# Performance work log

Measured on AMD Instinct MI355X. Metric: run time of the kernel, lower is better.

## Reference

```python
import jax, jax.numpy as jnp
import numpy as np

HIDDEN = 128
D_T = 128
D_S = 128
EPS = 1e-3  # keras LayerNormalization default epsilon


def setup_inputs() -> dict:
    key = jax.random.key(0)
    ks = jax.random.split(key, 9)
    B, S = 1024, 1024
    h_t = jax.random.normal(ks[0], (B, D_T), dtype=jnp.float32)
    h_s = jax.random.normal(ks[1], (B, S, D_S), dtype=jnp.float32)
    # Dense kernels (keras Dense: y = x @ W + b)
    W_a = jax.random.normal(ks[2], (D_T, HIDDEN), dtype=jnp.float32) * (1.0 / np.sqrt(D_T))
    U_a = jax.random.normal(ks[3], (D_S, HIDDEN), dtype=jnp.float32) * (1.0 / np.sqrt(D_S))
    V_a = jax.random.normal(ks[4], (HIDDEN, 1), dtype=jnp.float32) * (1.0 / np.sqrt(HIDDEN))
    W_c = jax.random.normal(ks[5], (D_S + D_T, HIDDEN), dtype=jnp.float32) * (1.0 / np.sqrt(D_S + D_T))
    b_c = jnp.zeros((HIDDEN,), dtype=jnp.float32)
    gamma = jnp.ones((HIDDEN,), dtype=jnp.float32)
    beta = jnp.zeros((HIDDEN,), dtype=jnp.float32)
    return {"h_t": h_t, "h_s": h_s, "W_a": W_a, "U_a": U_a, "V_a": V_a,
            "W_c": W_c, "b_c": b_c, "gamma": gamma, "beta": beta}


def reference(h_t, h_s, W_a, U_a, V_a, W_c, b_c, gamma, beta):
    # Additive (Bahdanau) attention scores
    ht_proj = h_t @ W_a                              # [B, H]
    hs_proj = jnp.einsum('bsd,dh->bsh', h_s, U_a)    # [B, S, H]
    energy = jnp.tanh(hs_proj + ht_proj[:, None, :])  # [B, S, H]
    scores = jnp.einsum('bsh,ho->bso', energy, V_a)  # [B, S, 1]
    alpha = jax.nn.softmax(scores, axis=1)           # softmax over sequence
    context = jnp.sum(alpha * h_s, axis=1)           # [B, D_S]
    concat = jnp.concatenate([context, h_t], axis=-1)  # [B, D_S + D_T]
    attn_vec = jnp.tanh(concat @ W_c + b_c)          # [B, H]
    # LayerNorm over last axis (keras default eps=1e-3)
    mu = jnp.mean(attn_vec, axis=-1, keepdims=True)
    var = jnp.mean(jnp.square(attn_vec - mu), axis=-1, keepdims=True)
    out = (attn_vec - mu) * jax.lax.rsqrt(var + EPS) * gamma + beta
    return out
```

## Files before the change

### kernel.cpp

```cpp
#include <hip/hip_runtime.h>

#define SEQ 1024
#define TS  64
#define NT  (SEQ/TS)

typedef unsigned short u16;
typedef unsigned int   u32;
typedef __bf16 bf16x8 __attribute__((ext_vector_type(8)));
typedef float  f32x4  __attribute__((ext_vector_type(4)));

__device__ __forceinline__ u16 f2bf(float f) {
    u32 u = __float_as_uint(f);
    u += 0x7fffu + ((u >> 16) & 1u);
    return (u16)(u >> 16);
}
__device__ __forceinline__ float bf2f(u16 h) {
    return __uint_as_float(((u32)h) << 16);
}
__device__ __forceinline__ float fast_tanh(float x) {
    float e = __expf(x + x);
    return 1.0f - 2.0f * __builtin_amdgcn_rcpf(e + 1.0f);
}

__global__ __launch_bounds__(256, 3)
void attn_fused(const float* __restrict__ h_t, const float* __restrict__ h_s,
                const float* __restrict__ W_a, const float* __restrict__ U_a,
                const float* __restrict__ V_a, const float* __restrict__ W_c,
                const float* __restrict__ b_c, const float* __restrict__ gamma,
                const float* __restrict__ beta, float* __restrict__ out)
{
    __shared__ u16 Ut[128*128];
    __shared__ u16 tileB[TS*128];
    __shared__ float htp[128];
    __shared__ float Vs[128];
    __shared__ float htrow[128];
    __shared__ float redArr[4*16];
    __shared__ float cw[4*128];
    __shared__ float mw[4], lw[4];
    __shared__ float lnp[4], lnq[4];

    const int tid = threadIdx.x;
    const int b   = blockIdx.x;
    const int w   = tid >> 6, l = tid & 63;
    const int lo  = l & 15,  hi = l >> 4;

    if (tid < 128) {
        htrow[tid] = h_t[b*128 + tid];
        Vs[tid]    = V_a[tid];
    }

    const float4* U4 = (const float4*)U_a;
    #pragma unroll
    for (int i = 0; i < 16; ++i) {
        int f4i = i*256 + tid;
        float4 v = U4[f4i];
        int k  = f4i >> 5;
        int cb = (f4i & 31) * 4;
        float vv[4] = {v.x, v.y, v.z, v.w};
        #pragma unroll
        for (int j = 0; j < 4; ++j) {
            int c = cb + j;
            Ut[c*128 + (((k>>3) ^ (c&7)) << 3) + (k&7)] = f2bf(vv[j]);
        }
    }
    __syncthreads();

    const float4* hs4 = (const float4*)h_s + (size_t)b * (SEQ*128/4);

    float4 rr[8];
    #pragma unroll
    for (int i = 0; i < 8; ++i) rr[i] = hs4[i*256 + tid];

    if (tid < 128) {
        float acc = 0.f;
        #pragma unroll 4
        for (int d = 0; d < 128; ++d) acc += htrow[d] * W_a[d*128 + tid];
        htp[tid] = acc;
    }

    #pragma unroll
    for (int i = 0; i < 8; ++i) {
        int f4i = i*256 + tid;
        int row = f4i >> 5, cf4 = f4i & 31;
        ushort4 pk = { f2bf(rr[i].x), f2bf(rr[i].y), f2bf(rr[i].z), f2bf(rr[i].w) };
        *(ushort4*)&tileB[row*128 + (((cf4>>1) ^ (row&7))<<3) + ((cf4&1)<<2)] = pk;
    }
    __syncthreads();

    float htpR[8], VsR[8];
    #pragma unroll
    for (int n = 0; n < 8; ++n) { htpR[n] = htp[n*16 + lo]; VsR[n] = Vs[n*16 + lo]; }

    const int swz = lo & 7;
    int aOff[4], bOff[4];
    #pragma unroll
    for (int ks = 0; ks < 4; ++ks) {
        int blk = (((ks*4 + hi) ^ swz) << 3);
        aOff[ks] = (w*16 + lo)*128 + blk;
        bOff[ks] = lo*128 + blk;
    }
    const int cblk   = l >> 2;
    const int ctxOff = (l & 3) << 1;

    float m = -1e30f, lsum = 0.f, c0 = 0.f, c1 = 0.f;

    for (int tt = 0; tt < NT; ++tt) {
        if (tt < NT-1) {
            #pragma unroll
            for (int i = 0; i < 8; ++i) rr[i] = hs4[(tt+1)*2048 + i*256 + tid];
        }

        bf16x8 a0 = *(const bf16x8*)&tileB[aOff[0]];
        bf16x8 a1 = *(const bf16x8*)&tileB[aOff[1]];
        bf16x8 a2 = *(const bf16x8*)&tileB[aOff[2]];
        bf16x8 a3 = *(const bf16x8*)&tileB[aOff[3]];
        float part0 = 0.f, part1 = 0.f, part2 = 0.f, part3 = 0.f;
        #pragma unroll
        for (int n = 0; n < 8; ++n) {
            f32x4 acc = {0.f, 0.f, 0.f, 0.f};
            acc = __builtin_amdgcn_mfma_f32_16x16x32_bf16(a0, *(const bf16x8*)&Ut[n*2048 + bOff[0]], acc, 0, 0, 0);
            acc = __builtin_amdgcn_mfma_f32_16x16x32_bf16(a1, *(const bf16x8*)&Ut[n*2048 + bOff[1]], acc, 0, 0, 0);
            acc = __builtin_amdgcn_mfma_f32_16x16x32_bf16(a2, *(const bf16x8*)&Ut[n*2048 + bOff[2]], acc, 0, 0, 0);
            acc = __builtin_amdgcn_mfma_f32_16x16x32_bf16(a3, *(const bf16x8*)&Ut[n*2048 + bOff[3]], acc, 0, 0, 0);
            float hC = htpR[n], vC = VsR[n];
            part0 += fast_tanh(acc[0] + hC) * vC;
            part1 += fast_tanh(acc[1] + hC) * vC;
            part2 += fast_tanh(acc[2] + hC) * vC;
            part3 += fast_tanh(acc[3] + hC) * vC;
        }
        #pragma unroll
        for (int msk = 1; msk < 16; msk <<= 1) {
            part0 += __shfl_xor(part0, msk);
            part1 += __shfl_xor(part1, msk);
            part2 += __shfl_xor(part2, msk);
            part3 += __shfl_xor(part3, msk);
        }
        float tm = fmaxf(fmaxf(part0, part1), fmaxf(part2, part3));
        tm = fmaxf(tm, __shfl_xor(tm, 16));
        tm = fmaxf(tm, __shfl_xor(tm, 32));
        float nm = fmaxf(m, tm);
        float sc = __expf(m - nm);
        c0 *= sc; c1 *= sc; lsum *= sc; m = nm;
        float w0 = __expf(part0 - m), w1 = __expf(part1 - m);
        float w2 = __expf(part2 - m), w3 = __expf(part3 - m);
        lsum += w0 + w1 + w2 + w3;
        if (lo == 0) {
            redArr[w*16 + hi*4 + 0] = w0;
            redArr[w*16 + hi*4 + 1] = w1;
            redArr[w*16 + hi*4 + 2] = w2;
            redArr[w*16 + hi*4 + 3] = w3;
        }
        #pragma unroll
        for (int r = 0; r < 16; ++r) {
            float wr = redArr[w*16 + r];
            u32 ud = *(const u32*)&tileB[(w*16 + r)*128 + ((cblk ^ (r&7)) << 3) + ctxOff];
            c0 += wr * bf2f((u16)(ud & 0xffffu));
            c1 += wr * bf2f((u16)(ud >> 16));
        }
        __syncthreads();
        if (tt < NT-1) {
            #pragma unroll
            for (int i = 0; i < 8; ++i) {
                int f4i = i*256 + tid;
                int row = f4i >> 5, cf4 = f4i & 31;
                ushort4 pk = { f2bf(rr[i].x), f2bf(rr[i].y), f2bf(rr[i].z), f2bf(rr[i].w) };
                *(ushort4*)&tileB[row*128 + (((cf4>>1) ^ (row&7))<<3) + ((cf4&1)<<2)] = pk;
            }
        }
        __syncthreads();
    }

    float lt = lsum;
    lt += __shfl_xor(lt, 16);
    lt += __shfl_xor(lt, 32);
    if (l == 0) { mw[w] = m; lw[w] = lt; }
    cw[w*128 + 2*l]     = c0;
    cw[w*128 + 2*l + 1] = c1;
    __syncthreads();

    if (tid < 128) {
        float M = fmaxf(fmaxf(mw[0], mw[1]), fmaxf(mw[2], mw[3]));
        float L = 0.f, C = 0.f;
        #pragma unroll
        for (int wv = 0; wv < 4; ++wv) {
            float s = __expf(mw[wv] - M);
            L += lw[wv] * s;
            C += cw[wv*128 + tid] * s;
        }
        htp[tid] = C / L;
    }
    __syncthreads();

    float av = 0.f;
    if (tid < 128) {
        float acc = b_c[tid];
        #pragma unroll 4
        for (int k = 0; k < 128; ++k) acc += htp[k]   * W_c[k*128 + tid];
        #pragma unroll 4
        for (int k = 0; k < 128; ++k) acc += htrow[k] * W_c[(128 + k)*128 + tid];
        av = fast_tanh(acc);
    }
    float s1 = (tid < 128) ? av : 0.f;
    #pragma unroll
    for (int msk = 1; msk < 64; msk <<= 1) s1 += __shfl_xor(s1, msk);
    if (l == 0) lnp[w] = s1;
    __syncthreads();
    float mu  = (lnp[0] + lnp[1]) * (1.f/128.f);
    float dev = av - mu;
    float s2 = (tid < 128) ? dev*dev : 0.f;
    #pragma unroll
    for (int msk = 1; msk < 64; msk <<= 1) s2 += __shfl_xor(s2, msk);
    if (l == 0) lnq[w] = s2;
    __syncthreads();
    float var = (lnq[0] + lnq[1]) * (1.f/128.f);
    if (tid < 128) {
        out[b*128 + tid] = dev * rsqrtf(var + 1e-3f) * gamma[tid] + beta[tid];
    }
}

extern "C" void kernel_launch(void* const* d_in, const int* in_sizes, int n_in,
                              void* d_out, int out_size, void* d_ws, size_t ws_size,
                              hipStream_t stream) {
    const float* h_t  = (const float*)d_in[0];
    const float* h_s  = (const float*)d_in[1];
    const float* W_a  = (const float*)d_in[2];
    const float* U_a  = (const float*)d_in[3];
    const float* V_a  = (const float*)d_in[4];
    const float* W_c  = (const float*)d_in[5];
    const float* b_c  = (const float*)d_in[6];
    const float* gam  = (const float*)d_in[7];
    const float* bet  = (const float*)d_in[8];
    float* out = (float*)d_out;
    hipLaunchKernelGGL(attn_fused, dim3(1024), dim3(256), 0, stream,
                       h_t, h_s, W_a, U_a, V_a, W_c, b_c, gam, bet, out);
}
```

Measured before the change: 155.8 us.

## Double-buffer h_s register prefetch two tiles ahead and use native bf16 conversion

Uses two register buffers for h_s tiles, loading each tile two iterations before it is committed to LDS, so global-load latency gets more compute time to hide behind. The loop is unrolled by two with macros. The manual float-to-bf16 rounding is replaced by the compiler's native __bf16 cast, which may map to hardware convert instructions. The extra 32 float registers per thread raise register pressure under the 3-blocks-per-SM launch bound and could cause spills or lower occupancy.

```diff
diff --git a/kernel.cpp b/kernel.cpp
--- a/kernel.cpp
+++ b/kernel.cpp
@@ -7,13 +7,9 @@
 typedef unsigned short u16;
 typedef unsigned int   u32;
 typedef __bf16 bf16x8 __attribute__((ext_vector_type(8)));
+typedef __bf16 bf16x4 __attribute__((ext_vector_type(4)));
 typedef float  f32x4  __attribute__((ext_vector_type(4)));
 
-__device__ __forceinline__ u16 f2bf(float f) {
-    u32 u = __float_as_uint(f);
-    u += 0x7fffu + ((u >> 16) & 1u);
-    return (u16)(u >> 16);
-}
 __device__ __forceinline__ float bf2f(u16 h) {
     return __uint_as_float(((u32)h) << 16);
 }
@@ -21,6 +17,76 @@
     float e = __expf(x + x);
     return 1.0f - 2.0f * __builtin_amdgcn_rcpf(e + 1.0f);
 }
+
+#define LOADT(rr, tt)                                                   \
+    do {                                                                \
+        _Pragma("unroll")                                               \
+        for (int i = 0; i < 8; ++i) rr[i] = hs4[(tt)*2048 + i*256 + tid]; \
+    } while (0)
+
+#define COMMIT(rr)                                                      \
+    do {                                                                \
+        _Pragma("unroll")                                               \
+        for (int i = 0; i < 8; ++i) {                                   \
+            int f4i = i*256 + tid;                                      \
+            int row = f4i >> 5, cf4 = f4i & 31;                         \
+            bf16x4 pk;                                                  \
+            pk[0] = (__bf16)rr[i].x; pk[1] = (__bf16)rr[i].y;           \
+            pk[2] = (__bf16)rr[i].z; pk[3] = (__bf16)rr[i].w;           \
+            *(bf16x4*)&tileB[row*128 + (((cf4>>1) ^ (row&7))<<3) + ((cf4&1)<<2)] = pk; \
+        }                                                               \
+    } while (0)
+
+#define COMPUTE()                                                       \
+    do {                                                                \
+        bf16x8 a0 = *(const bf16x8*)&tileB[aOff[0]];                    \
+        bf16x8 a1 = *(const bf16x8*)&tileB[aOff[1]];                    \
+        bf16x8 a2 = *(const bf16x8*)&tileB[aOff[2]];                    \
+        bf16x8 a3 = *(const bf16x8*)&tileB[aOff[3]];                    \
+        float part0 = 0.f, part1 = 0.f, part2 = 0.f, part3 = 0.f;       \
+        _Pragma("unroll")                                               \
+        for (int n = 0; n < 8; ++n) {                                   \
+            f32x4 acc = {0.f, 0.f, 0.f, 0.f};                           \
+            acc = __builtin_amdgcn_mfma_f32_16x16x32_bf16(a0, *(const bf16x8*)&Ut[n*2048 + bOff[0]], acc, 0, 0, 0); \
+            acc = __builtin_amdgcn_mfma_f32_16x16x32_bf16(a1, *(const bf16x8*)&Ut[n*2048 + bOff[1]], acc, 0, 0, 0); \
+            acc = __builtin_amdgcn_mfma_f32_16x16x32_bf16(a2, *(const bf16x8*)&Ut[n*2048 + bOff[2]], acc, 0, 0, 0); \
+            acc = __builtin_amdgcn_mfma_f32_16x16x32_bf16(a3, *(const bf16x8*)&Ut[n*2048 + bOff[3]], acc, 0, 0, 0); \
+            float hC = htpR[n], vC = VsR[n];                            \
+            part0 += fast_tanh(acc[0] + hC) * vC;                       \
+            part1 += fast_tanh(acc[1] + hC) * vC;                       \
+            part2 += fast_tanh(acc[2] + hC) * vC;                       \
+            part3 += fast_tanh(acc[3] + hC) * vC;                       \
+        }                                                               \
+        _Pragma("unroll")                                               \
+        for (int msk = 1; msk < 16; msk <<= 1) {                        \
+            part0 += __shfl_xor(part0, msk);                            \
+            part1 += __shfl_xor(part1, msk);                            \
+            part2 += __shfl_xor(part2, msk);                            \
+            part3 += __shfl_xor(part3, msk);                            \
+        }                                                               \
+        float tm = fmaxf(fmaxf(part0, part1), fmaxf(part2, part3));     \
+        tm = fmaxf(tm, __shfl_xor(tm, 16));                             \
+        tm = fmaxf(tm, __shfl_xor(tm, 32));                             \
+        float nm = fmaxf(m, tm);                                        \
+        float sc = __expf(m - nm);                                      \
+        c0 *= sc; c1 *= sc; lsum *= sc; m = nm;                         \
+        float w0 = __expf(part0 - m), w1 = __expf(part1 - m);           \
+        float w2 = __expf(part2 - m), w3 = __expf(part3 - m);           \
+        lsum += w0 + w1 + w2 + w3;                                      \
+        if (lo == 0) {                                                  \
+            redArr[w*16 + hi*4 + 0] = w0;                               \
+            redArr[w*16 + hi*4 + 1] = w1;                               \
+            redArr[w*16 + hi*4 + 2] = w2;                               \
+            redArr[w*16 + hi*4 + 3] = w3;                               \
+        }                                                               \
+        _Pragma("unroll")                                               \
+        for (int r = 0; r < 16; ++r) {                                  \
+            float wr = redArr[w*16 + r];                                \
+            u32 ud = *(const u32*)&tileB[(w*16 + r)*128 + ((cblk ^ (r&7)) << 3) + ctxOff]; \
+            c0 += wr * bf2f((u16)(ud & 0xffffu));                       \
+            c1 += wr * bf2f((u16)(ud >> 16));                           \
+        }                                                               \
+    } while (0)
 
 __global__ __launch_bounds__(256, 3)
 void attn_fused(const float* __restrict__ h_t, const float* __restrict__ h_s,
@@ -60,16 +126,16 @@
         #pragma unroll
         for (int j = 0; j < 4; ++j) {
             int c = cb + j;
-            Ut[c*128 + (((k>>3) ^ (c&7)) << 3) + (k&7)] = f2bf(vv[j]);
+            Ut[c*128 + (((k>>3) ^ (c&7)) << 3) + (k&7)] = __builtin_bit_cast(u16, (__bf16)vv[j]);
         }
     }
     __syncthreads();
 
     const float4* hs4 = (const float4*)h_s + (size_t)b * (SEQ*128/4);
 
-    float4 rr[8];
-    #pragma unroll
-    for (int i = 0; i < 8; ++i) rr[i] = hs4[i*256 + tid];
+    float4 rrA[8], rrB[8];
+    LOADT(rrA, 0);
+    LOADT(rrB, 1);
 
     if (tid < 128) {
         float acc = 0.f;
@@ -78,13 +144,7 @@
         htp[tid] = acc;
     }
 
-    #pragma unroll
-    for (int i = 0; i < 8; ++i) {
-        int f4i = i*256 + tid;
-        int row = f4i >> 5, cf4 = f4i & 31;
-        ushort4 pk = { f2bf(rr[i].x), f2bf(rr[i].y), f2bf(rr[i].z), f2bf(rr[i].w) };
-        *(ushort4*)&tileB[row*128 + (((cf4>>1) ^ (row&7))<<3) + ((cf4&1)<<2)] = pk;
-    }
+    COMMIT(rrA);
     __syncthreads();
 
     float htpR[8], VsR[8];
@@ -104,69 +164,17 @@
 
     float m = -1e30f, lsum = 0.f, c0 = 0.f, c1 = 0.f;
 
-    for (int tt = 0; tt < NT; ++tt) {
-        if (tt < NT-1) {
-            #pragma unroll
-            for (int i = 0; i < 8; ++i) rr[i] = hs4[(tt+1)*2048 + i*256 + tid];
-        }
-
-        bf16x8 a0 = *(const bf16x8*)&tileB[aOff[0]];
-        bf16x8 a1 = *(const bf16x8*)&tileB[aOff[1]];
-        bf16x8 a2 = *(const bf16x8*)&tileB[aOff[2]];
-        bf16x8 a3 = *(const bf16x8*)&tileB[aOff[3]];
-        float part0 = 0.f, part1 = 0.f, part2 = 0.f, part3 = 0.f;
-        #pragma unroll
-        for (int n = 0; n < 8; ++n) {
-            f32x4 acc = {0.f, 0.f, 0.f, 0.f};
-            acc = __builtin_amdgcn_mfma_f32_16x16x32_bf16(a0, *(const bf16x8*)&Ut[n*2048 + bOff[0]], acc, 0, 0, 0);
-            acc = __builtin_amdgcn_mfma_f32_16x16x32_bf16(a1, *(const bf16x8*)&Ut[n*2048 + bOff[1]], acc, 0, 0, 0);
-            acc = __builtin_amdgcn_mfma_f32_16x16x32_bf16(a2, *(const bf16x8*)&Ut[n*2048 + bOff[2]], acc, 0, 0, 0);
-            acc = __builtin_amdgcn_mfma_f32_16x16x32_bf16(a3, *(const bf16x8*)&Ut[n*2048 + bOff[3]], acc, 0, 0, 0);
-            float hC = htpR[n], vC = VsR[n];
-            part0 += fast_tanh(acc[0] + hC) * vC;
-            part1 += fast_tanh(acc[1] + hC) * vC;
-            part2 += fast_tanh(acc[2] + hC) * vC;
-            part3 += fast_tanh(acc[3] + hC) * vC;
-        }
-        #pragma unroll
-        for (int msk = 1; msk < 16; msk <<= 1) {
-            part0 += __shfl_xor(part0, msk);
-            part1 += __shfl_xor(part1, msk);
-            part2 += __shfl_xor(part2, msk);
-            part3 += __shfl_xor(part3, msk);
-        }
-        float tm = fmaxf(fmaxf(part0, part1), fmaxf(part2, part3));
-        tm = fmaxf(tm, __shfl_xor(tm, 16));
-        tm = fmaxf(tm, __shfl_xor(tm, 32));
-        float nm = fmaxf(m, tm);
-        float sc = __expf(m - nm);
-        c0 *= sc; c1 *= sc; lsum *= sc; m = nm;
-        float w0 = __expf(part0 - m), w1 = __expf(part1 - m);
-        float w2 = __expf(part2 - m), w3 = __expf(part3 - m);
-        lsum += w0 + w1 + w2 + w3;
-        if (lo == 0) {
-            redArr[w*16 + hi*4 + 0] = w0;
-            redArr[w*16 + hi*4 + 1] = w1;
-            redArr[w*16 + hi*4 + 2] = w2;
-            redArr[w*16 + hi*4 + 3] = w3;
-        }
-        #pragma unroll
-        for (int r = 0; r < 16; ++r) {
-            float wr = redArr[w*16 + r];
-            u32 ud = *(const u32*)&tileB[(w*16 + r)*128 + ((cblk ^ (r&7)) << 3) + ctxOff];
-            c0 += wr * bf2f((u16)(ud & 0xffffu));
-            c1 += wr * bf2f((u16)(ud >> 16));
-        }
-        __syncthreads();
-        if (tt < NT-1) {
-            #pragma unroll
-            for (int i = 0; i < 8; ++i) {
-                int f4i = i*256 + tid;
-                int row = f4i >> 5, cf4 = f4i & 31;
-                ushort4 pk = { f2bf(rr[i].x), f2bf(rr[i].y), f2bf(rr[i].z), f2bf(rr[i].w) };
-                *(ushort4*)&tileB[row*128 + (((cf4>>1) ^ (row&7))<<3) + ((cf4&1)<<2)] = pk;
-            }
-        }
+    for (int t = 0; t < NT; t += 2) {
+        if (t + 2 < NT) LOADT(rrA, t + 2);
+        COMPUTE();
+        __syncthreads();
+        COMMIT(rrB);
+        __syncthreads();
+
+        if (t + 3 < NT) LOADT(rrB, t + 3);
+        COMPUTE();
+        __syncthreads();
+        if (t + 2 < NT) COMMIT(rrA);
         __syncthreads();
     }
 
```

Result: slower. 368.6 us (+136.6%).

## Hold U_a fragments in registers and double-buffer per-wave h_s tiles without barriers

Applied to the files above, without the earlier changes.

Each thread now keeps its slice of the U_a MFMA B-operand in registers as bf16 fragments, so the 32 KB shared-memory copy of U_a and its per-tile LDS reads go away. Each wave loads and stores only its own 16 rows of h_s into a double-buffered shared tile, which removes both __syncthreads from the main loop. The bf16 conversion uses the native cast instead of manual rounding. The cost is much higher register pressure (launch bounds lowered from 3 to 2 blocks per CU) and strided uncoalesced global reads of U_a per block.

```diff
diff --git a/kernel.cpp b/kernel.cpp
--- a/kernel.cpp
+++ b/kernel.cpp
@@ -1,19 +1,15 @@
 #include <hip/hip_runtime.h>
 
 #define SEQ 1024
-#define TS  64
-#define NT  (SEQ/TS)
+#define NT  16
+#define TILE_U16 (64*128)
 
 typedef unsigned short u16;
 typedef unsigned int   u32;
 typedef __bf16 bf16x8 __attribute__((ext_vector_type(8)));
+typedef __bf16 bf16x4 __attribute__((ext_vector_type(4)));
 typedef float  f32x4  __attribute__((ext_vector_type(4)));
 
-__device__ __forceinline__ u16 f2bf(float f) {
-    u32 u = __float_as_uint(f);
-    u += 0x7fffu + ((u >> 16) & 1u);
-    return (u16)(u >> 16);
-}
 __device__ __forceinline__ float bf2f(u16 h) {
     return __uint_as_float(((u32)h) << 16);
 }
@@ -22,54 +18,120 @@
     return 1.0f - 2.0f * __builtin_amdgcn_rcpf(e + 1.0f);
 }
 
-__global__ __launch_bounds__(256, 3)
+#define LOADT(rr, tt)                                                       \
+    do {                                                                    \
+        _Pragma("unroll")                                                   \
+        for (int i = 0; i < 8; ++i)                                         \
+            rr[i] = hs4[(tt)*2048 + w*512 + i*64 + l];                      \
+    } while (0)
+
+#define COMMIT(rr, sel)                                                     \
+    do {                                                                    \
+        _Pragma("unroll")                                                   \
+        for (int i = 0; i < 8; ++i) {                                       \
+            int f4i = i*64 + l;                                             \
+            int r   = w*16 + (f4i >> 5);                                    \
+            int cf4 = f4i & 31;                                             \
+            bf16x4 pk;                                                      \
+            pk[0] = (__bf16)rr[i].x; pk[1] = (__bf16)rr[i].y;               \
+            pk[2] = (__bf16)rr[i].z; pk[3] = (__bf16)rr[i].w;               \
+            *(bf16x4*)&tileB[(sel)*TILE_U16 + r*128 +                       \
+                             (((cf4>>1) ^ (r&7))<<3) + ((cf4&1)<<2)] = pk;  \
+        }                                                                   \
+    } while (0)
+
+#define COMPUTE(sel)                                                        \
+    do {                                                                    \
+        const u16* tb = &tileB[(sel)*TILE_U16];                             \
+        bf16x8 a0 = *(const bf16x8*)&tb[aOff[0]];                           \
+        bf16x8 a1 = *(const bf16x8*)&tb[aOff[1]];                           \
+        bf16x8 a2 = *(const bf16x8*)&tb[aOff[2]];                           \
+        bf16x8 a3 = *(const bf16x8*)&tb[aOff[3]];                           \
+        float part0 = 0.f, part1 = 0.f, part2 = 0.f, part3 = 0.f;           \
+        _Pragma("unroll")                                                   \
+        for (int n = 0; n < 8; ++n) {                                       \
+            f32x4 acc = {0.f, 0.f, 0.f, 0.f};                               \
+            acc = __builtin_amdgcn_mfma_f32_16x16x32_bf16(a0, Bf[n][0], acc, 0, 0, 0); \
+            acc = __builtin_amdgcn_mfma_f32_16x16x32_bf16(a1, Bf[n][1], acc, 0, 0, 0); \
+            acc = __builtin_amdgcn_mfma_f32_16x16x32_bf16(a2, Bf[n][2], acc, 0, 0, 0); \
+            acc = __builtin_amdgcn_mfma_f32_16x16x32_bf16(a3, Bf[n][3], acc, 0, 0, 0); \
+            float hC = htpR[n], vC = VsR[n];                                \
+            part0 += fast_tanh(acc[0] + hC) * vC;                           \
+            part1 += fast_tanh(acc[1] + hC) * vC;                           \
+            part2 += fast_tanh(acc[2] + hC) * vC;                           \
+            part3 += fast_tanh(acc[3] + hC) * vC;                           \
+        }                                                                   \
+        _Pragma("unroll")                                                   \
+        for (int msk = 1; msk < 16; msk <<= 1) {                            \
+            part0 += __shfl_xor(part0, msk);                                \
+            part1 += __shfl_xor(part1, msk);                                \
+            part2 += __shfl_xor(part2, msk);                                \
+            part3 += __shfl_xor(part3, msk);                                \
+        }                                                                   \
+        float tm = fmaxf(fmaxf(part0, part1), fmaxf(part2, part3));         \
+        tm = fmaxf(tm, __shfl_xor(tm, 16));                                 \
+        tm = fmaxf(tm, __shfl_xor(tm, 32));                                 \
+        float nm = fmaxf(m, tm);                                            \
+        float sc = __expf(m - nm);                                          \
+        c0 *= sc; c1 *= sc; lsum *= sc; m = nm;                             \
+        float w0 = __expf(part0 - m), w1 = __expf(part1 - m);               \
+        float w2 = __expf(part2 - m), w3 = __expf(part3 - m);               \
+        lsum += w0 + w1 + w2 + w3;                                          \
+        if (lo == 0) {                                                      \
+            redArr[w*16 + hi*4 + 0] = w0;                                   \
+            redArr[w*16 + hi*4 + 1] = w1;                                   \
+            redArr[w*16 + hi*4 + 2] = w2;                                   \
+            redArr[w*16 + hi*4 + 3] = w3;                                   \
+        }                                                                   \
+        _Pragma("unroll")                                                   \
+        for (int r = 0; r < 16; ++r) {                                      \
+            float wr = redArr[w*16 + r];                                    \
+            u32 ud = *(const u32*)&tb[(w*16 + r)*128 +                      \
+                                      ((cblk ^ (r&7)) << 3) + ctxOff];      \
+            c0 += wr * bf2f((u16)(ud & 0xffffu));                           \
+            c1 += wr * bf2f((u16)(ud >> 16));                               \
+        }                                                                   \
+    } while (0)
+
+__global__ __launch_bounds__(256, 2)
 void attn_fused(const float* __restrict__ h_t, const float* __restrict__ h_s,
                 const float* __restrict__ W_a, const float* __restrict__ U_a,
                 const float* __restrict__ V_a, const float* __restrict__ W_c,
                 const float* __restrict__ b_c, const float* __restrict__ gamma,
                 const float* __restrict__ beta, float* __restrict__ out)
 {
-    __shared__ u16 Ut[128*128];
-    __shared__ u16 tileB[TS*128];
+    __shared__ u16 tileB[2*TILE_U16];
     __shared__ float htp[128];
-    __shared__ float Vs[128];
     __shared__ float htrow[128];
     __shared__ float redArr[4*16];
     __shared__ float cw[4*128];
-    __shared__ float mw[4], lw[4];
-    __shared__ float lnp[4], lnq[4];
+    __shared__ float mw[4], lw[4], lnp[4], lnq[4];
 
     const int tid = threadIdx.x;
     const int b   = blockIdx.x;
     const int w   = tid >> 6, l = tid & 63;
     const int lo  = l & 15,  hi = l >> 4;
 
-    if (tid < 128) {
-        htrow[tid] = h_t[b*128 + tid];
-        Vs[tid]    = V_a[tid];
-    }
-
-    const float4* U4 = (const float4*)U_a;
-    #pragma unroll
-    for (int i = 0; i < 16; ++i) {
-        int f4i = i*256 + tid;
-        float4 v = U4[f4i];
-        int k  = f4i >> 5;
-        int cb = (f4i & 31) * 4;
-        float vv[4] = {v.x, v.y, v.z, v.w};
+    const float4* hs4 = (const float4*)h_s + (size_t)b * (SEQ*32);
+
+    float4 rr[8];
+    LOADT(rr, 0);
+
+    bf16x8 Bf[8][4];
+    #pragma unroll
+    for (int n = 0; n < 8; ++n) {
         #pragma unroll
-        for (int j = 0; j < 4; ++j) {
-            int c = cb + j;
-            Ut[c*128 + (((k>>3) ^ (c&7)) << 3) + (k&7)] = f2bf(vv[j]);
+        for (int ks = 0; ks < 4; ++ks) {
+            bf16x8 f;
+            #pragma unroll
+            for (int j = 0; j < 8; ++j)
+                f[j] = (__bf16)U_a[(ks*32 + hi*8 + j)*128 + n*16 + lo];
+            Bf[n][ks] = f;
         }
     }
-    __syncthreads();
-
-    const float4* hs4 = (const float4*)h_s + (size_t)b * (SEQ*128/4);
-
-    float4 rr[8];
-    #pragma unroll
-    for (int i = 0; i < 8; ++i) rr[i] = hs4[i*256 + tid];
+
+    if (tid < 128) htrow[tid] = h_t[b*128 + tid];
+    __syncthreads();
 
     if (tid < 128) {
         float acc = 0.f;
@@ -77,105 +139,35 @@
         for (int d = 0; d < 128; ++d) acc += htrow[d] * W_a[d*128 + tid];
         htp[tid] = acc;
     }
-
-    #pragma unroll
-    for (int i = 0; i < 8; ++i) {
-        int f4i = i*256 + tid;
-        int row = f4i >> 5, cf4 = f4i & 31;
-        ushort4 pk = { f2bf(rr[i].x), f2bf(rr[i].y), f2bf(rr[i].z), f2bf(rr[i].w) };
-        *(ushort4*)&tileB[row*128 + (((cf4>>1) ^ (row&7))<<3) + ((cf4&1)<<2)] = pk;
-    }
+    COMMIT(rr, 0);
     __syncthreads();
 
     float htpR[8], VsR[8];
     #pragma unroll
-    for (int n = 0; n < 8; ++n) { htpR[n] = htp[n*16 + lo]; VsR[n] = Vs[n*16 + lo]; }
+    for (int n = 0; n < 8; ++n) { htpR[n] = htp[n*16 + lo]; VsR[n] = V_a[n*16 + lo]; }
 
     const int swz = lo & 7;
-    int aOff[4], bOff[4];
-    #pragma unroll
-    for (int ks = 0; ks < 4; ++ks) {
-        int blk = (((ks*4 + hi) ^ swz) << 3);
-        aOff[ks] = (w*16 + lo)*128 + blk;
-        bOff[ks] = lo*128 + blk;
-    }
+    int aOff[4];
+    #pragma unroll
+    for (int ks = 0; ks < 4; ++ks)
+        aOff[ks] = (w*16 + lo)*128 + (((ks*4 + hi) ^ swz) << 3);
     const int cblk   = l >> 2;
     const int ctxOff = (l & 3) << 1;
 
     float m = -1e30f, lsum = 0.f, c0 = 0.f, c1 = 0.f;
 
-    for (int tt = 0; tt < NT; ++tt) {
-        if (tt < NT-1) {
-            #pragma unroll
-            for (int i = 0; i < 8; ++i) rr[i] = hs4[(tt+1)*2048 + i*256 + tid];
-        }
-
-        bf16x8 a0 = *(const bf16x8*)&tileB[aOff[0]];
-        bf16x8 a1 = *(const bf16x8*)&tileB[aOff[1]];
-        bf16x8 a2 = *(const bf16x8*)&tileB[aOff[2]];
-        bf16x8 a3 = *(const bf16x8*)&tileB[aOff[3]];
-        float part0 = 0.f, part1 = 0.f, part2 = 0.f, part3 = 0.f;
-        #pragma unroll
-        for (int n = 0; n < 8; ++n) {
-            f32x4 acc = {0.f, 0.f, 0.f, 0.f};
-            acc = __builtin_amdgcn_mfma_f32_16x16x32_bf16(a0, *(const bf16x8*)&Ut[n*2048 + bOff[0]], acc, 0, 0, 0);
-            acc = __builtin_amdgcn_mfma_f32_16x16x32_bf16(a1, *(const bf16x8*)&Ut[n*2048 + bOff[1]], acc, 0, 0, 0);
-            acc = __builtin_amdgcn_mfma_f32_16x16x32_bf16(a2, *(const bf16x8*)&Ut[n*2048 + bOff[2]], acc, 0, 0, 0);
-            acc = __builtin_amdgcn_mfma_f32_16x16x32_bf16(a3, *(const bf16x8*)&Ut[n*2048 + bOff[3]], acc, 0, 0, 0);
-            float hC = htpR[n], vC = VsR[n];
-            part0 += fast_tanh(acc[0] + hC) * vC;
-            part1 += fast_tanh(acc[1] + hC) * vC;
-            part2 += fast_tanh(acc[2] + hC) * vC;
-            part3 += fast_tanh(acc[3] + hC) * vC;
-        }
-        #pragma unroll
-        for (int msk = 1; msk < 16; msk <<= 1) {
-            part0 += __shfl_xor(part0, msk);
-            part1 += __shfl_xor(part1, msk);
-            part2 += __shfl_xor(part2, msk);
-            part3 += __shfl_xor(part3, msk);
-        }
-        float tm = fmaxf(fmaxf(part0, part1), fmaxf(part2, part3));
-        tm = fmaxf(tm, __shfl_xor(tm, 16));
-        tm = fmaxf(tm, __shfl_xor(tm, 32));
-        float nm = fmaxf(m, tm);
-        float sc = __expf(m - nm);
-        c0 *= sc; c1 *= sc; lsum *= sc; m = nm;
-        float w0 = __expf(part0 - m), w1 = __expf(part1 - m);
-        float w2 = __expf(part2 - m), w3 = __expf(part3 - m);
-        lsum += w0 + w1 + w2 + w3;
-        if (lo == 0) {
-            redArr[w*16 + hi*4 + 0] = w0;
-            redArr[w*16 + hi*4 + 1] = w1;
-            redArr[w*16 + hi*4 + 2] = w2;
-            redArr[w*16 + hi*4 + 3] = w3;
-        }
-        #pragma unroll
-        for (int r = 0; r < 16; ++r) {
-            float wr = redArr[w*16 + r];
-            u32 ud = *(const u32*)&tileB[(w*16 + r)*128 + ((cblk ^ (r&7)) << 3) + ctxOff];
-            c0 += wr * bf2f((u16)(ud & 0xffffu));
-            c1 += wr * bf2f((u16)(ud >> 16));
-        }
-        __syncthreads();
-        if (tt < NT-1) {
-            #pragma unroll
-            for (int i = 0; i < 8; ++i) {
-                int f4i = i*256 + tid;
-                int row = f4i >> 5, cf4 = f4i & 31;
-                ushort4 pk = { f2bf(rr[i].x), f2bf(rr[i].y), f2bf(rr[i].z), f2bf(rr[i].w) };
-                *(ushort4*)&tileB[row*128 + (((cf4>>1) ^ (row&7))<<3) + ((cf4&1)<<2)] = pk;
-            }
-        }
-        __syncthreads();
-    }
+    for (int t = 0; t < NT-1; ++t) {
+        LOADT(rr, t+1);
+        COMPUTE(t & 1);
+        COMMIT(rr, (t+1) & 1);
+    }
+    COMPUTE((NT-1) & 1);
 
     float lt = lsum;
     lt += __shfl_xor(lt, 16);
     lt += __shfl_xor(lt, 32);
     if (l == 0) { mw[w] = m; lw[w] = lt; }
-    cw[w*128 + 2*l]     = c0;
-    cw[w*128 + 2*l + 1] = c1;
+    *(float2*)&cw[w*128 + 2*l] = make_float2(c0, c1);
     __syncthreads();
 
     if (tid < 128) {
```

Result: slower. 347.8 us (+123.3%).
